# Optimization experiments

Hardware: AMD Instinct MI355X
Metric: run time of the kernel (lower is better)

## Reference

```python
import jax, jax.numpy as jnp
import numpy as np

B, S, D = 4, 2048, 1024

def setup_inputs() -> dict:
    key = jax.random.key(0)
    kv, kk, kq, kw = jax.random.split(key, 4)
    scale = 1.0 / np.sqrt(D)
    v = jax.random.normal(kv, (B, S, D), dtype=jnp.float32)
    k = jax.random.normal(kk, (B, S, D), dtype=jnp.float32)
    q = jax.random.normal(kq, (B, S, D), dtype=jnp.float32)
    wi = jax.random.normal(kw, (D, D), dtype=jnp.float32) * scale
    mask = jnp.tril(jnp.ones((S, S), dtype=bool))[None, :, :]  # causal [1,S,S]
    return {"v": v, "k": k, "q": q, "wi": wi, "mask": mask}

def reference(v, k, q, wi, mask):
    # project q, k, v with the shared weight wi
    q = q @ wi
    k = k @ wi
    v = v @ wi
    # scaled dot-product scores [B,S,S]
    scores = jnp.einsum('bqd,bkd->bqk', q, k) / jnp.sqrt(jnp.asarray(q.shape[-1], q.dtype))
    scores = jnp.where(mask, scores, jnp.asarray(-1e10, scores.dtype))
    attn = jax.nn.softmax(scores, axis=-1)
    # residual: q + attn @ v
    return q + jnp.einsum('bqk,bkd->bqd', attn, v)
```

## Files before the change

kernel.cpp:

```cpp
#include <hip/hip_runtime.h>
#include <hip/hip_bf16.h>

typedef __hip_bfloat16 bf16;
typedef short bf16x8 __attribute__((ext_vector_type(8)));
typedef float f32x4 __attribute__((ext_vector_type(4)));

#define HT 16384

__device__ __forceinline__ void gload16(const void* g, void* l) {
    __builtin_amdgcn_global_load_lds(
        (const __attribute__((address_space(1))) void*)g,
        (__attribute__((address_space(3))) void*)l, 16, 0, 0);
}

__device__ __forceinline__ void stage_half(char* lds, const bf16* src, int ld,
                                           int rowbase, int k0, int slotIdx,
                                           int tid)
{
    char* dst = lds + (size_t)slotIdx * HT + tid * 16;
    const int sub = tid >> 3;
    const int cb  = ((tid & 7) ^ (sub & 7)) << 4;
    #pragma unroll
    for (int p = 0; p < 2; ++p) {
        const int row = p * 64 + sub;
        const char* g = (const char*)(src + (size_t)(rowbase + row) * ld + k0) + cb;
        gload16(g, dst + p * 8192);
    }
}

__device__ __forceinline__ bf16x8 ldsfrag(const char* lds, int slotIdx,
                                          int row, int ks, int cb0)
{
    return *(const bf16x8*)(lds + (size_t)slotIdx * HT
                            + row * 128 + (cb0 ^ (ks << 6)));
}

__device__ __forceinline__ void stage_Af32(char* base, const float* src,
                                           int rowbase, int k0, int slot, int tid)
{
    char* dst = base + slot * 32768 + tid * 16;
    #pragma unroll
    for (int p = 0; p < 4; ++p) {
        const int s = p * 512 + tid;
        const int row = s >> 4, ch = s & 15;
        const char* g = (const char*)(src + (size_t)(rowbase + row) * 1024 + k0)
                        + ((ch ^ (row & 15)) << 4);
        gload16(g, dst + p * 8192);
    }
}

__device__ __forceinline__ bf16x8 fragAf32(const char* base, int slot,
                                           int row, int ks, int fq)
{
    const char* p0 = base + slot * 32768 + row * 256;
    const int c0 = ks * 8 + fq * 2, r15 = row & 15;
    f32x4 lo = *(const f32x4*)(p0 + ((c0 ^ r15) << 4));
    f32x4 hi = *(const f32x4*)(p0 + (((c0 + 1) ^ r15) << 4));
    union { short h[8]; bf16x8 v; } o;
    #pragma unroll
    for (int e = 0; e < 4; ++e) {
        bf16 a = __float2bfloat16(lo[e]), b = __float2bfloat16(hi[e]);
        o.h[e] = *(short*)&a;
        o.h[4 + e] = *(short*)&b;
    }
    return o.v;
}

__launch_bounds__(512, 2)
__global__ void proj_f32(const float* __restrict__ q, const float* __restrict__ k,
                         const float* __restrict__ v, const bf16* __restrict__ B,
                         bf16* __restrict__ C)
{
    extern __shared__ char lds[];
    const int orig = blockIdx.y * 8 + blockIdx.x;
    const int wk = (orig & 7) * 96 + (orig >> 3);
    const int bi = wk >> 3, bj = wk & 7;
    const int brow = bi * 256, bcol = bj * 128;
    const float* Asrc = (bi < 32) ? q : (bi < 64) ? k : v;
    const int arow = (bi & 31) * 256;

    const int tid  = threadIdx.x;
    const int lane = tid & 63;
    const int w    = tid >> 6;
    const int wm   = w >> 1, wn = w & 1;
    const int fr   = lane & 15, fq = lane >> 4;
    const int cb0  = ((fr & 7) ^ fq) << 4;
    const int slotA = wm >> 1;
    const int rA    = (wm & 1) * 64;
    const int rB    = wn * 64;
    const int NT    = 16;

    f32x4 acc[4][4] = {};
    bf16x8 af[4][2], bv[4][2];

#define BBASE(buf) (lds + (buf) * 81920 + 65536)
#define ABASE(buf) (lds + (buf) * 81920)
#define STAGE_B(buf, k0)                                                      \
    {                                                                         \
        char* dst_ = BBASE(buf) + tid * 16;                                   \
        const int sub_ = tid >> 3;                                            \
        const int cb_  = ((tid & 7) ^ (sub_ & 7)) << 4;                       \
        _Pragma("unroll") for (int p_ = 0; p_ < 2; ++p_) {                    \
            const int row_ = p_ * 64 + sub_;                                  \
            const char* g_ = (const char*)(B + (size_t)(bcol + row_) * 1024   \
                                           + (k0)) + cb_;                     \
            gload16(g_, dst_ + p_ * 8192);                                    \
        }                                                                     \
    }

    STAGE_B(0, 0)
    stage_Af32(ABASE(0), Asrc, arow,      0, 0, tid);
    stage_Af32(ABASE(0), Asrc, arow + 128, 0, 1, tid);
    STAGE_B(1, 64)
    asm volatile("s_waitcnt vmcnt(2)" ::: "memory");
    __builtin_amdgcn_s_barrier();

#define QUAD2(m0, n0)                                                         \
    _Pragma("unroll") for (int dm = 0; dm < 2; ++dm)                          \
    _Pragma("unroll") for (int dn = 0; dn < 2; ++dn)                          \
    _Pragma("unroll") for (int ks = 0; ks < 2; ++ks)                          \
        acc[(m0)+dm][(n0)+dn] = __builtin_amdgcn_mfma_f32_16x16x32_bf16(      \
            af[(m0)+dm][ks], bv[(n0)+dn][ks], acc[(m0)+dm][(n0)+dn], 0, 0, 0);

    for (int t = 0; t < NT; ++t) {
        const int buf = t & 1, nbuf = buf ^ 1;
        const int k1 = min(t + 1, NT - 1) << 6;
        const int k2 = min(t + 2, NT - 1) << 6;

        #pragma unroll
        for (int m = 0; m < 2; ++m)
            #pragma unroll
            for (int ks = 0; ks < 2; ++ks)
                af[m][ks] = fragAf32(ABASE(buf), slotA, rA + m * 16 + fr, ks, fq);
        #pragma unroll
        for (int n = 0; n < 2; ++n)
            #pragma unroll
            for (int ks = 0; ks < 2; ++ks)
                bv[n][ks] = ldsfrag(BBASE(buf), 0, rB + n * 16 + fr, ks, cb0);
        stage_Af32(ABASE(nbuf), Asrc, arow, k1, 0, tid);
        __builtin_amdgcn_s_barrier();
        __builtin_amdgcn_s_setprio(1);
        QUAD2(0, 0)
        __builtin_amdgcn_s_setprio(0);
        __builtin_amdgcn_s_barrier();

        #pragma unroll
        for (int n = 2; n < 4; ++n)
            #pragma unroll
            for (int ks = 0; ks < 2; ++ks)
                bv[n][ks] = ldsfrag(BBASE(buf), 0, rB + n * 16 + fr, ks, cb0);
        stage_Af32(ABASE(nbuf), Asrc, arow + 128, k1, 1, tid);
        __builtin_amdgcn_s_barrier();
        __builtin_amdgcn_s_setprio(1);
        QUAD2(0, 2)
        __builtin_amdgcn_s_setprio(0);
        __builtin_amdgcn_s_barrier();

        #pragma unroll
        for (int m = 2; m < 4; ++m)
            #pragma unroll
            for (int ks = 0; ks < 2; ++ks)
                af[m][ks] = fragAf32(ABASE(buf), slotA, rA + m * 16 + fr, ks, fq);
        STAGE_B(buf, k2)
        __builtin_amdgcn_s_barrier();
        __builtin_amdgcn_s_setprio(1);
        QUAD2(2, 2)
        __builtin_amdgcn_s_setprio(0);
        __builtin_amdgcn_s_barrier();

        __builtin_amdgcn_s_setprio(1);
        QUAD2(2, 0)
        __builtin_amdgcn_s_setprio(0);
        asm volatile("s_waitcnt vmcnt(2)" ::: "memory");
        __builtin_amdgcn_s_barrier();
    }
#undef QUAD2
#undef STAGE_B
#undef ABASE
#undef BBASE

    #pragma unroll
    for (int mf = 0; mf < 4; ++mf) {
        const int r0 = brow + wm * 64 + mf * 16 + fq * 4;
        #pragma unroll
        for (int nf = 0; nf < 4; ++nf) {
            const int c = bcol + wn * 64 + nf * 16 + fr;
            #pragma unroll
            for (int j = 0; j < 4; ++j)
                C[(size_t)(r0 + j) * 1024 + c] = __float2bfloat16(acc[mf][nf][j]);
        }
    }
}

template<int MODE>
__launch_bounds__(512, 2)
__global__ void gemm_bn128(const bf16* __restrict__ A, const bf16* __restrict__ B,
                           bf16* __restrict__ Cb, float* __restrict__ Cf,
                           const bf16* __restrict__ Res,
                           int lda, int ldb, int ldc, int K,
                           long sA, long sB, long sC, long sR, float scale)
{
    extern __shared__ char lds[];
    int bi, bj;
    if (MODE == 1) { bj = blockIdx.x; bi = blockIdx.y; if (bj > 2 * bi + 1) return; }
    else           { bi = blockIdx.x; bj = blockIdx.y; }
    const int bz = blockIdx.z;
    A += (size_t)bz * sA;
    B += (size_t)bz * sB;
    const int brow = bi * 256, bcol = bj * 128;

    const int tid  = threadIdx.x;
    const int lane = tid & 63;
    const int w    = tid >> 6;
    const int wm   = w >> 1, wn = w & 1;
    const int fr   = lane & 15, fq = lane >> 4;
    const int cb0  = ((fr & 7) ^ fq) << 4;
    const int slotA = wm >> 1;
    const int rA    = (wm & 1) * 64;
    const int rB    = wn * 64;

    const int kmax = (MODE == 2) ? (brow + 256) : K;
    const int NT   = kmax >> 6;

    f32x4 acc[4][4] = {};
    bf16x8 af[4][2], bv[4][2];

    stage_half(lds, B, ldb, bcol,       0, 2, tid);
    stage_half(lds, A, lda, brow,       0, 0, tid);
    stage_half(lds, A, lda, brow + 128, 0, 1, tid);
    stage_half(lds, B, ldb, bcol,      64, 5, tid);
    asm volatile("s_waitcnt vmcnt(2)" ::: "memory");
    __builtin_amdgcn_s_barrier();

#define QUAD2(m0, n0)                                                         \
    _Pragma("unroll") for (int dm = 0; dm < 2; ++dm)                          \
    _Pragma("unroll") for (int dn = 0; dn < 2; ++dn)                          \
    _Pragma("unroll") for (int ks = 0; ks < 2; ++ks)                          \
        acc[(m0)+dm][(n0)+dn] = __builtin_amdgcn_mfma_f32_16x16x32_bf16(      \
            af[(m0)+dm][ks], bv[(n0)+dn][ks], acc[(m0)+dm][(n0)+dn], 0, 0, 0);

    for (int t = 0; t < NT; ++t) {
        const int buf = t & 1, nbuf = buf ^ 1;
        const int k1 = min(t + 1, NT - 1) << 6;
        const int k2 = min(t + 2, NT - 1) << 6;

        #pragma unroll
        for (int m = 0; m < 2; ++m)
            #pragma unroll
            for (int ks = 0; ks < 2; ++ks)
                af[m][ks] = ldsfrag(lds, buf * 3 + slotA, rA + m * 16 + fr, ks, cb0);
        #pragma unroll
        for (int n = 0; n < 2; ++n)
            #pragma unroll
            for (int ks = 0; ks < 2; ++ks)
                bv[n][ks] = ldsfrag(lds, buf * 3 + 2, rB + n * 16 + fr, ks, cb0);
        stage_half(lds, A, lda, brow, k1, nbuf * 3 + 0, tid);
        __builtin_amdgcn_s_barrier();
        __builtin_amdgcn_s_setprio(1);
        QUAD2(0, 0)
        __builtin_amdgcn_s_setprio(0);
        __builtin_amdgcn_s_barrier();

        #pragma unroll
        for (int n = 2; n < 4; ++n)
            #pragma unroll
            for (int ks = 0; ks < 2; ++ks)
                bv[n][ks] = ldsfrag(lds, buf * 3 + 2, rB + n * 16 + fr, ks, cb0);
        stage_half(lds, A, lda, brow + 128, k1, nbuf * 3 + 1, tid);
        __builtin_amdgcn_s_barrier();
        __builtin_amdgcn_s_setprio(1);
        QUAD2(0, 2)
        __builtin_amdgcn_s_setprio(0);
        __builtin_amdgcn_s_barrier();

        #pragma unroll
        for (int m = 2; m < 4; ++m)
            #pragma unroll
            for (int ks = 0; ks < 2; ++ks)
                af[m][ks] = ldsfrag(lds, buf * 3 + slotA, rA + m * 16 + fr, ks, cb0);
        stage_half(lds, B, ldb, bcol, k2, buf * 3 + 2, tid);
        __builtin_amdgcn_s_barrier();
        __builtin_amdgcn_s_setprio(1);
        QUAD2(2, 2)
        __builtin_amdgcn_s_setprio(0);
        __builtin_amdgcn_s_barrier();

        __builtin_amdgcn_s_setprio(1);
        QUAD2(2, 0)
        __builtin_amdgcn_s_setprio(0);
        asm volatile("s_waitcnt vmcnt(2)" ::: "memory");
        __builtin_amdgcn_s_barrier();
    }
#undef QUAD2

    if (MODE == 1) {
        bf16* C = Cb + (size_t)bz * sC;
        #pragma unroll
        for (int mf = 0; mf < 4; ++mf) {
            const int r0 = brow + wm * 64 + mf * 16 + fq * 4;
            #pragma unroll
            for (int nf = 0; nf < 4; ++nf) {
                const int c = bcol + wn * 64 + nf * 16 + fr;
                #pragma unroll
                for (int j = 0; j < 4; ++j)
                    C[(size_t)(r0 + j) * ldc + c] =
                        __float2bfloat16(acc[mf][nf][j] * scale);
            }
        }
    } else {
        float* C = Cf + (size_t)bz * sC;
        const bf16* R = Res + (size_t)bz * sR;
        #pragma unroll
        for (int mf = 0; mf < 4; ++mf) {
            const int r0 = brow + wm * 64 + mf * 16 + fq * 4;
            #pragma unroll
            for (int nf = 0; nf < 4; ++nf) {
                const int c = bcol + wn * 64 + nf * 16 + fr;
                #pragma unroll
                for (int j = 0; j < 4; ++j)
                    C[(size_t)(r0 + j) * ldc + c] = acc[mf][nf][j] +
                        __bfloat162float(R[(size_t)(r0 + j) * ldc + c]);
            }
        }
    }
}

__global__ void transpose_wi(const float* __restrict__ wi, bf16* __restrict__ Wt)
{
    __shared__ float t[32][33];
    const int n0 = blockIdx.x * 32, k0 = blockIdx.y * 32;
    const int lx = threadIdx.x & 31, ly = threadIdx.x >> 5;
    for (int i = ly; i < 32; i += 8)
        t[i][lx] = wi[(size_t)(k0 + i) * 1024 + n0 + lx];
    __syncthreads();
    for (int i = ly; i < 32; i += 8)
        Wt[(size_t)(n0 + i) * 1024 + k0 + lx] = __float2bfloat16(t[lx][i]);
}

__global__ void transpose_vp(const bf16* __restrict__ vp, bf16* __restrict__ vpT)
{
    __shared__ bf16 t[32][33];
    const int b = blockIdx.z;
    const int d0 = blockIdx.x * 32, s0 = blockIdx.y * 32;
    const bf16* src = vp + (size_t)b * 2048 * 1024;
    bf16* dst = vpT + (size_t)b * 1024 * 2048;
    const int lx = threadIdx.x & 31, ly = threadIdx.x >> 5;
    for (int i = ly; i < 32; i += 8)
        t[i][lx] = src[(size_t)(s0 + i) * 1024 + d0 + lx];
    __syncthreads();
    for (int i = ly; i < 32; i += 8)
        dst[(size_t)(d0 + i) * 2048 + s0 + lx] = t[lx][i];
}

__device__ __forceinline__ float bf2f(short s) {
    union { float f; unsigned u; } c;
    c.u = ((unsigned)(unsigned short)s) << 16;
    return c.f;
}

__launch_bounds__(256)
__global__ void softmax_rows(bf16* __restrict__ P)
{
    const int wid = threadIdx.x >> 6, lane = threadIdx.x & 63;
    const int r = blockIdx.x * 4 + wid, b = blockIdx.y;
    bf16* row = P + ((size_t)b * 2048 + r) * 2048;
    const int nv  = r + 1;
    const int rup = (r & ~255) + 256;

    float vals[4][8];
    float m = -1e30f;
    #pragma unroll
    for (int c = 0; c < 4; ++c) {
        const int k0 = c * 512 + lane * 8;
        if (k0 < rup) {
            bf16x8 x = *(const bf16x8*)(row + k0);
            #pragma unroll
            for (int j = 0; j < 8; ++j) {
                float f = (k0 + j < nv) ? bf2f(x[j]) : -1e30f;
                vals[c][j] = f;
                m = fmaxf(m, f);
            }
        } else {
            #pragma unroll
            for (int j = 0; j < 8; ++j) vals[c][j] = -1e30f;
        }
    }
    #pragma unroll
    for (int o = 32; o; o >>= 1) m = fmaxf(m, __shfl_xor(m, o));

    float sum = 0.f;
    #pragma unroll
    for (int c = 0; c < 4; ++c)
        #pragma unroll
        for (int j = 0; j < 8; ++j) {
            float e = __expf(vals[c][j] - m);
            vals[c][j] = e;
            sum += e;
        }
    #pragma unroll
    for (int o = 32; o; o >>= 1) sum += __shfl_xor(sum, o);
    const float inv = 1.0f / sum;

    #pragma unroll
    for (int c = 0; c < 4; ++c) {
        const int k0 = c * 512 + lane * 8;
        if (k0 < rup) {
            union { short h[8]; bf16x8 v8; } o;
            #pragma unroll
            for (int j = 0; j < 8; ++j) {
                bf16 hh = __float2bfloat16(vals[c][j] * inv);
                o.h[j] = *(short*)&hh;
            }
            *(bf16x8*)(row + k0) = o.v8;
        }
    }
}

extern "C" void kernel_launch(void* const* d_in, const int* in_sizes, int n_in,
                              void* d_out, int out_size, void* d_ws, size_t ws_size,
                              hipStream_t stream)
{
    const float* v  = (const float*)d_in[0];
    const float* k  = (const float*)d_in[1];
    const float* q  = (const float*)d_in[2];
    const float* wi = (const float*)d_in[3];
    float* out = (float*)d_out;

    char* ws = (char*)d_ws;
    const size_t WT_OFF   = 0;
    const size_t PROJ_OFF = WT_OFF + (2u << 20);
    const size_t VPT_OFF  = PROJ_OFF + (size_t)24576 * 1024 * 2;
    const size_t P_OFF    = VPT_OFF + (size_t)4 * 1024 * 2048 * 2;

    bf16* Wt   = (bf16*)(ws + WT_OFF);
    bf16* proj = (bf16*)(ws + PROJ_OFF);
    bf16* vpT  = (bf16*)(ws + VPT_OFF);
    bf16* P    = (bf16*)(ws + P_OFF);

    bf16* qp_b = proj;
    bf16* kp_b = proj + (size_t)8192 * 1024;
    bf16* vp_b = proj + (size_t)16384 * 1024;

    (void)hipFuncSetAttribute((const void*)proj_f32,
            hipFuncAttributeMaxDynamicSharedMemorySize, 163840);
    (void)hipFuncSetAttribute((const void*)gemm_bn128<1>,
            hipFuncAttributeMaxDynamicSharedMemorySize, 98304);
    (void)hipFuncSetAttribute((const void*)gemm_bn128<2>,
            hipFuncAttributeMaxDynamicSharedMemorySize, 98304);

    transpose_wi<<<dim3(32, 32), 256, 0, stream>>>(wi, Wt);

    proj_f32<<<dim3(8, 96), 512, 163840, stream>>>(q, k, v, Wt, proj);

    transpose_vp<<<dim3(32, 64, 4), 256, 0, stream>>>(vp_b, vpT);

    gemm_bn128<1><<<dim3(16, 8, 4), 512, 98304, stream>>>(
        qp_b, kp_b, P, nullptr, nullptr,
        1024, 1024, 2048, 1024,
        (long)2048 * 1024, (long)2048 * 1024, (long)2048 * 2048, 0, 0.03125f);

    softmax_rows<<<dim3(512, 4), 256, 0, stream>>>(P);

    gemm_bn128<2><<<dim3(8, 8, 4), 512, 98304, stream>>>(
        P, vpT, nullptr, out, qp_b,
        2048, 2048, 1024, 2048,
        (long)2048 * 2048, (long)1024 * 2048, (long)2048 * 1024, (long)2048 * 1024, 1.0f);
}
```

Baseline: 183.8 us.

## Convert fp32 activations to bf16 via registers and skip masked blocks in PV GEMM

The projection kernel now loads fp32 activation tiles into registers, converts them to bf16 once, and writes swizzled bf16 tiles to LDS. This replaces staging fp32 in LDS and converting on every fragment read, which cuts LDS footprint and per-fragment conversion work. The P@V GEMM is replaced by a causal-aware kernel that only iterates K up to the diagonal block. Each workgroup pairs tile i with tile 15-i to balance the triangular work, using a 3-slot ring for P. This risks new load/LDS ordering hazards, from register-staged writes and manual vmcnt counts, in exchange for skipping the fully masked upper triangle.

```diff
diff --git a/kernel.cpp b/kernel.cpp
--- a/kernel.cpp
+++ b/kernel.cpp
@@ -35,41 +35,16 @@
                             + row * 128 + (cb0 ^ (ks << 6)));
 }
 
-__device__ __forceinline__ void stage_Af32(char* base, const float* src,
-                                           int rowbase, int k0, int slot, int tid)
-{
-    char* dst = base + slot * 32768 + tid * 16;
-    #pragma unroll
-    for (int p = 0; p < 4; ++p) {
-        const int s = p * 512 + tid;
-        const int row = s >> 4, ch = s & 15;
-        const char* g = (const char*)(src + (size_t)(rowbase + row) * 1024 + k0)
-                        + ((ch ^ (row & 15)) << 4);
-        gload16(g, dst + p * 8192);
-    }
-}
-
-__device__ __forceinline__ bf16x8 fragAf32(const char* base, int slot,
-                                           int row, int ks, int fq)
-{
-    const char* p0 = base + slot * 32768 + row * 256;
-    const int c0 = ks * 8 + fq * 2, r15 = row & 15;
-    f32x4 lo = *(const f32x4*)(p0 + ((c0 ^ r15) << 4));
-    f32x4 hi = *(const f32x4*)(p0 + (((c0 + 1) ^ r15) << 4));
-    union { short h[8]; bf16x8 v; } o;
-    #pragma unroll
-    for (int e = 0; e < 4; ++e) {
-        bf16 a = __float2bfloat16(lo[e]), b = __float2bfloat16(hi[e]);
-        o.h[e] = *(short*)&a;
-        o.h[4 + e] = *(short*)&b;
-    }
-    return o.v;
+__device__ __forceinline__ float bf2f(short s) {
+    union { float f; unsigned u; } c;
+    c.u = ((unsigned)(unsigned short)s) << 16;
+    return c.f;
 }
 
 __launch_bounds__(512, 2)
-__global__ void proj_f32(const float* __restrict__ q, const float* __restrict__ k,
-                         const float* __restrict__ v, const bf16* __restrict__ B,
-                         bf16* __restrict__ C)
+__global__ void proj_fused(const float* __restrict__ q, const float* __restrict__ k,
+                           const float* __restrict__ v, const bf16* __restrict__ B,
+                           bf16* __restrict__ C)
 {
     extern __shared__ char lds[];
     const int orig = blockIdx.y * 8 + blockIdx.x;
@@ -90,29 +65,46 @@
     const int rB    = wn * 64;
     const int NT    = 16;
 
+    const int sh    = tid >> 8;
+    const int ss    = tid & 255;
+    const int srow  = ss >> 1;
+    const int spart = ss & 1;
+    const float* gbase = Asrc + (size_t)(arow + sh * 128 + srow) * 1024 + spart * 32;
+
     f32x4 acc[4][4] = {};
     bf16x8 af[4][2], bv[4][2];
-
-#define BBASE(buf) (lds + (buf) * 81920 + 65536)
-#define ABASE(buf) (lds + (buf) * 81920)
-#define STAGE_B(buf, k0)                                                      \
+    float4 ld[8];
+
+#define LOADA(kk)                                                             \
+    _Pragma("unroll") for (int j = 0; j < 8; ++j)                             \
+        ld[j] = *(const float4*)(gbase + (kk) + j * 4);
+
+#define WRITEA(nb)                                                            \
     {                                                                         \
-        char* dst_ = BBASE(buf) + tid * 16;                                   \
-        const int sub_ = tid >> 3;                                            \
-        const int cb_  = ((tid & 7) ^ (sub_ & 7)) << 4;                       \
-        _Pragma("unroll") for (int p_ = 0; p_ < 2; ++p_) {                    \
-            const int row_ = p_ * 64 + sub_;                                  \
-            const char* g_ = (const char*)(B + (size_t)(bcol + row_) * 1024   \
-                                           + (k0)) + cb_;                     \
-            gload16(g_, dst_ + p_ * 8192);                                    \
+        char* hbase = lds + (size_t)((nb) * 3 + sh) * HT + srow * 128;        \
+        _Pragma("unroll") for (int c = 0; c < 4; ++c) {                       \
+            union { short h[8]; bf16x8 v8; } o_;                              \
+            float4 a_ = ld[2 * c], b_ = ld[2 * c + 1];                        \
+            bf16 t0 = __float2bfloat16(a_.x), t1 = __float2bfloat16(a_.y),    \
+                 t2 = __float2bfloat16(a_.z), t3 = __float2bfloat16(a_.w),    \
+                 t4 = __float2bfloat16(b_.x), t5 = __float2bfloat16(b_.y),    \
+                 t6 = __float2bfloat16(b_.z), t7 = __float2bfloat16(b_.w);    \
+            o_.h[0] = *(short*)&t0; o_.h[1] = *(short*)&t1;                   \
+            o_.h[2] = *(short*)&t2; o_.h[3] = *(short*)&t3;                   \
+            o_.h[4] = *(short*)&t4; o_.h[5] = *(short*)&t5;                   \
+            o_.h[6] = *(short*)&t6; o_.h[7] = *(short*)&t7;                   \
+            *(bf16x8*)(hbase + (((spart * 4 + c) ^ (srow & 7)) << 4)) = o_.v8;\
         }                                                                     \
     }
 
-    STAGE_B(0, 0)
-    stage_Af32(ABASE(0), Asrc, arow,      0, 0, tid);
-    stage_Af32(ABASE(0), Asrc, arow + 128, 0, 1, tid);
-    STAGE_B(1, 64)
-    asm volatile("s_waitcnt vmcnt(2)" ::: "memory");
+    LOADA(0)
+    asm volatile("s_waitcnt vmcnt(0)" ::: "memory");
+    WRITEA(0)
+    stage_half(lds, B, 1024, bcol, 0, 2, tid);
+    LOADA(64)
+    stage_half(lds, B, 1024, bcol, 64, 5, tid);
+    asm volatile("s_waitcnt vmcnt(10)" ::: "memory");
+    asm volatile("s_waitcnt lgkmcnt(0)" ::: "memory");
     __builtin_amdgcn_s_barrier();
 
 #define QUAD2(m0, n0)                                                         \
@@ -124,20 +116,21 @@
 
     for (int t = 0; t < NT; ++t) {
         const int buf = t & 1, nbuf = buf ^ 1;
-        const int k1 = min(t + 1, NT - 1) << 6;
         const int k2 = min(t + 2, NT - 1) << 6;
 
         #pragma unroll
         for (int m = 0; m < 2; ++m)
             #pragma unroll
             for (int ks = 0; ks < 2; ++ks)
-                af[m][ks] = fragAf32(ABASE(buf), slotA, rA + m * 16 + fr, ks, fq);
+                af[m][ks] = ldsfrag(lds, buf * 3 + slotA, rA + m * 16 + fr, ks, cb0);
         #pragma unroll
         for (int n = 0; n < 2; ++n)
             #pragma unroll
             for (int ks = 0; ks < 2; ++ks)
-                bv[n][ks] = ldsfrag(BBASE(buf), 0, rB + n * 16 + fr, ks, cb0);
-        stage_Af32(ABASE(nbuf), Asrc, arow, k1, 0, tid);
+                bv[n][ks] = ldsfrag(lds, buf * 3 + 2, rB + n * 16 + fr, ks, cb0);
+        asm volatile("s_waitcnt vmcnt(2)" ::: "memory");
+        WRITEA(nbuf)
+        LOADA(k2)
         __builtin_amdgcn_s_barrier();
         __builtin_amdgcn_s_setprio(1);
         QUAD2(0, 0)
@@ -148,8 +141,7 @@
         for (int n = 2; n < 4; ++n)
             #pragma unroll
             for (int ks = 0; ks < 2; ++ks)
-                bv[n][ks] = ldsfrag(BBASE(buf), 0, rB + n * 16 + fr, ks, cb0);
-        stage_Af32(ABASE(nbuf), Asrc, arow + 128, k1, 1, tid);
+                bv[n][ks] = ldsfrag(lds, buf * 3 + 2, rB + n * 16 + fr, ks, cb0);
         __builtin_amdgcn_s_barrier();
         __builtin_amdgcn_s_setprio(1);
         QUAD2(0, 2)
@@ -160,8 +152,8 @@
         for (int m = 2; m < 4; ++m)
             #pragma unroll
             for (int ks = 0; ks < 2; ++ks)
-                af[m][ks] = fragAf32(ABASE(buf), slotA, rA + m * 16 + fr, ks, fq);
-        STAGE_B(buf, k2)
+                af[m][ks] = ldsfrag(lds, buf * 3 + slotA, rA + m * 16 + fr, ks, cb0);
+        stage_half(lds, B, 1024, bcol, k2, buf * 3 + 2, tid);
         __builtin_amdgcn_s_barrier();
         __builtin_amdgcn_s_setprio(1);
         QUAD2(2, 2)
@@ -171,13 +163,13 @@
         __builtin_amdgcn_s_setprio(1);
         QUAD2(2, 0)
         __builtin_amdgcn_s_setprio(0);
-        asm volatile("s_waitcnt vmcnt(2)" ::: "memory");
+        asm volatile("s_waitcnt vmcnt(10)" ::: "memory");
+        asm volatile("s_waitcnt lgkmcnt(0)" ::: "memory");
         __builtin_amdgcn_s_barrier();
     }
 #undef QUAD2
-#undef STAGE_B
-#undef ABASE
-#undef BBASE
+#undef LOADA
+#undef WRITEA
 
     #pragma unroll
     for (int mf = 0; mf < 4; ++mf) {
@@ -294,7 +286,7 @@
 #undef QUAD2
 
     if (MODE == 1) {
-        bf16* C = Cb + (size_t)bz * sC;
+        bf16* Co = Cb + (size_t)bz * sC;
         #pragma unroll
         for (int mf = 0; mf < 4; ++mf) {
             const int r0 = brow + wm * 64 + mf * 16 + fq * 4;
@@ -303,12 +295,12 @@
                 const int c = bcol + wn * 64 + nf * 16 + fr;
                 #pragma unroll
                 for (int j = 0; j < 4; ++j)
-                    C[(size_t)(r0 + j) * ldc + c] =
+                    Co[(size_t)(r0 + j) * ldc + c] =
                         __float2bfloat16(acc[mf][nf][j] * scale);
             }
         }
     } else {
-        float* C = Cf + (size_t)bz * sC;
+        float* Co = Cf + (size_t)bz * sC;
         const bf16* R = Res + (size_t)bz * sR;
         #pragma unroll
         for (int mf = 0; mf < 4; ++mf) {
@@ -318,11 +310,116 @@
                 const int c = bcol + wn * 64 + nf * 16 + fr;
                 #pragma unroll
                 for (int j = 0; j < 4; ++j)
-                    C[(size_t)(r0 + j) * ldc + c] = acc[mf][nf][j] +
+                    Co[(size_t)(r0 + j) * ldc + c] = acc[mf][nf][j] +
                         __bfloat162float(R[(size_t)(r0 + j) * ldc + c]);
             }
         }
     }
+}
+
+__device__ __forceinline__ void pv_tile(char* lds, const bf16* P, const bf16* V,
+                                        const bf16* R, float* C, int bi, int bcol,
+                                        int tid, int wm, int wn, int fr, int fq,
+                                        int cb0)
+{
+    const int brow = bi * 128;
+    const int NT = 2 * (bi + 1);
+    f32x4 acc[4][2] = {};
+    bf16x8 af[4][2], bv[2][2];
+
+    stage_half(lds, P, 2048, brow, 0,  0, tid);
+    stage_half(lds, V, 2048, bcol, 0,  3, tid);
+    stage_half(lds, P, 2048, brow, 64, 1, tid);
+    stage_half(lds, V, 2048, bcol, 64, 4, tid);
+    asm volatile("s_waitcnt vmcnt(4)" ::: "memory");
+    __builtin_amdgcn_s_barrier();
+
+    for (int t = 0; t < NT; ++t) {
+        const int aslot = t % 3, bslot = 3 + (t & 1);
+        const int k2 = min(t + 2, NT - 1) << 6;
+
+        #pragma unroll
+        for (int m = 0; m < 2; ++m)
+            #pragma unroll
+            for (int ks = 0; ks < 2; ++ks)
+                af[m][ks] = ldsfrag(lds, aslot, wm * 64 + m * 16 + fr, ks, cb0);
+        #pragma unroll
+        for (int n = 0; n < 2; ++n)
+            #pragma unroll
+            for (int ks = 0; ks < 2; ++ks)
+                bv[n][ks] = ldsfrag(lds, bslot, wn * 32 + n * 16 + fr, ks, cb0);
+        stage_half(lds, P, 2048, brow, k2, (t + 2) % 3, tid);
+        __builtin_amdgcn_s_barrier();
+        __builtin_amdgcn_s_setprio(1);
+        #pragma unroll
+        for (int m = 0; m < 2; ++m)
+            #pragma unroll
+            for (int n = 0; n < 2; ++n)
+                #pragma unroll
+                for (int ks = 0; ks < 2; ++ks)
+                    acc[m][n] = __builtin_amdgcn_mfma_f32_16x16x32_bf16(
+                        af[m][ks], bv[n][ks], acc[m][n], 0, 0, 0);
+        __builtin_amdgcn_s_setprio(0);
+        __builtin_amdgcn_s_barrier();
+
+        #pragma unroll
+        for (int m = 2; m < 4; ++m)
+            #pragma unroll
+            for (int ks = 0; ks < 2; ++ks)
+                af[m][ks] = ldsfrag(lds, aslot, wm * 64 + m * 16 + fr, ks, cb0);
+        stage_half(lds, V, 2048, bcol, k2, bslot, tid);
+        __builtin_amdgcn_s_barrier();
+        __builtin_amdgcn_s_setprio(1);
+        #pragma unroll
+        for (int m = 2; m < 4; ++m)
+            #pragma unroll
+            for (int n = 0; n < 2; ++n)
+                #pragma unroll
+                for (int ks = 0; ks < 2; ++ks)
+                    acc[m][n] = __builtin_amdgcn_mfma_f32_16x16x32_bf16(
+                        af[m][ks], bv[n][ks], acc[m][n], 0, 0, 0);
+        __builtin_amdgcn_s_setprio(0);
+        asm volatile("s_waitcnt vmcnt(4)" ::: "memory");
+        __builtin_amdgcn_s_barrier();
+    }
+
+    #pragma unroll
+    for (int mf = 0; mf < 4; ++mf) {
+        const int r0 = brow + wm * 64 + mf * 16 + fq * 4;
+        #pragma unroll
+        for (int nf = 0; nf < 2; ++nf) {
+            const int c = bcol + wn * 32 + nf * 16 + fr;
+            #pragma unroll
+            for (int j = 0; j < 4; ++j)
+                C[(size_t)(r0 + j) * 1024 + c] = acc[mf][nf][j] +
+                    __bfloat162float(R[(size_t)(r0 + j) * 1024 + c]);
+        }
+    }
+}
+
+__launch_bounds__(512, 4)
+__global__ void pv128(const bf16* __restrict__ P, const bf16* __restrict__ V,
+                      const bf16* __restrict__ R, float* __restrict__ C)
+{
+    extern __shared__ char lds[];
+    const int pid = blockIdx.x, bj = blockIdx.y, bz = blockIdx.z;
+    const bf16* Pb = P + (size_t)bz * 2048 * 2048;
+    const bf16* Vb = V + (size_t)bz * 1024 * 2048;
+    const bf16* Rb = R + (size_t)bz * 2048 * 1024;
+    float* Cb = C + (size_t)bz * 2048 * 1024;
+
+    const int tid  = threadIdx.x;
+    const int lane = tid & 63;
+    const int w    = tid >> 6;
+    const int wm   = w >> 2, wn = w & 3;
+    const int fr   = lane & 15, fq = lane >> 4;
+    const int cb0  = ((fr & 7) ^ fq) << 4;
+    const int bcol = bj * 128;
+
+    pv_tile(lds, Pb, Vb, Rb, Cb, pid, bcol, tid, wm, wn, fr, fq, cb0);
+    asm volatile("s_waitcnt vmcnt(0) lgkmcnt(0)" ::: "memory");
+    __builtin_amdgcn_s_barrier();
+    pv_tile(lds, Pb, Vb, Rb, Cb, 15 - pid, bcol, tid, wm, wn, fr, fq, cb0);
 }
 
 __global__ void transpose_wi(const float* __restrict__ wi, bf16* __restrict__ Wt)
@@ -352,12 +449,6 @@
         dst[(size_t)(d0 + i) * 2048 + s0 + lx] = t[lx][i];
 }
 
-__device__ __forceinline__ float bf2f(short s) {
-    union { float f; unsigned u; } c;
-    c.u = ((unsigned)(unsigned short)s) << 16;
-    return c.f;
-}
-
 __launch_bounds__(256)
 __global__ void softmax_rows(bf16* __restrict__ P)
 {
@@ -441,16 +532,16 @@
     bf16* kp_b = proj + (size_t)8192 * 1024;
     bf16* vp_b = proj + (size_t)16384 * 1024;
 
-    (void)hipFuncSetAttribute((const void*)proj_f32,
-            hipFuncAttributeMaxDynamicSharedMemorySize, 163840);
+    (void)hipFuncSetAttribute((const void*)proj_fused,
+            hipFuncAttributeMaxDynamicSharedMemorySize, 98304);
     (void)hipFuncSetAttribute((const void*)gemm_bn128<1>,
             hipFuncAttributeMaxDynamicSharedMemorySize, 98304);
-    (void)hipFuncSetAttribute((const void*)gemm_bn128<2>,
-            hipFuncAttributeMaxDynamicSharedMemorySize, 98304);
+    (void)hipFuncSetAttribute((const void*)pv128,
+            hipFuncAttributeMaxDynamicSharedMemorySize, 81920);
 
     transpose_wi<<<dim3(32, 32), 256, 0, stream>>>(wi, Wt);
 
-    proj_f32<<<dim3(8, 96), 512, 163840, stream>>>(q, k, v, Wt, proj);
+    proj_fused<<<dim3(8, 96), 512, 98304, stream>>>(q, k, v, Wt, proj);
 
     transpose_vp<<<dim3(32, 64, 4), 256, 0, stream>>>(vp_b, vpT);
 
@@ -461,8 +552,5 @@
 
     softmax_rows<<<dim3(512, 4), 256, 0, stream>>>(P);
 
-    gemm_bn128<2><<<dim3(8, 8, 4), 512, 98304, stream>>>(
-        P, vpT, nullptr, out, qp_b,
-        2048, 2048, 1024, 2048,
-        (long)2048 * 2048, (long)1024 * 2048, (long)2048 * 1024, (long)2048 * 1024, 1.0f);
-}
+    pv128<<<dim3(8, 8, 4), 512, 81920, stream>>>(P, vpT, qp_b, out);
+}
```

After: 228.0 us. +24.0%, slower.
